# Kernel tuning notes

Hardware: AMD Instinct MI355X
Metric: run time of the kernel (lower is better)

Reference implementation:

```python
import jax, jax.numpy as jnp
import numpy as np

B_IN, B_L1, B_L2 = 64, 16, 8
F1, F2, F_OUT = 64, 128, 10
BATCH = 16
CPLX = jnp.complex64

# ---------- numpy precompute: quadrature weights, Wigner-d matrices, grids ----------

def _dh_weights(b):
    # Driscoll-Healy quadrature weights over the 2b beta samples
    j = np.arange(2 * b)
    l = np.arange(b)
    s = np.sin(np.outer(2 * j + 1, 2 * l + 1) * np.pi / (4 * b)) @ (1.0 / (2 * l + 1))
    return ((2.0 / b) * np.sin(np.pi * (2 * j + 1) / (4 * b)) * s).astype(np.float32)

def _wigner_d_all(lmax, betas):
    # d^l(beta) = exp(-i beta Jy) via eigendecomposition of Jy (quantum convention)
    betas = np.asarray(betas, np.float64)
    out = []
    for l in range(lmax + 1):
        m = np.arange(-l, l)
        cp = np.sqrt(l * (l + 1) - m * (m + 1))
        Jy = np.zeros((2 * l + 1, 2 * l + 1), np.complex128)
        Jy[np.arange(1, 2 * l + 1), np.arange(0, 2 * l)] = -0.5j * cp
        Jy[np.arange(0, 2 * l), np.arange(1, 2 * l + 1)] = 0.5j * cp
        lam, V = np.linalg.eigh(Jy)
        ph = np.exp(-1j * np.outer(betas, lam))
        d = np.einsum('mk,bk,nk->bmn', V, ph, V.conj())
        out.append(np.ascontiguousarray(d.real.astype(np.float32)))
    return out

def _s2_grid():
    beta = np.arange(1, 4) * (np.pi / 8) / 3
    alpha = np.linspace(0, 2 * np.pi, 8, endpoint=False)
    B, A = np.meshgrid(beta, alpha, indexing='ij')
    return B.ravel(), A.ravel()

def _so3_grid():
    beta = np.arange(1, 4) * (np.pi / 8) / 3
    alpha = np.linspace(0, 2 * np.pi, 8, endpoint=False)
    pre_gamma = np.linspace(0, 2 * np.pi, 8, endpoint=False)
    B, A, C = np.meshgrid(beta, alpha, pre_gamma, indexing='ij')
    return B.ravel(), A.ravel(), (C - A).ravel()

_BETAS_IN = np.pi * (2 * np.arange(2 * B_IN) + 1) / (4 * B_IN)
_BETAS_L1 = np.pi * (2 * np.arange(2 * B_L1) + 1) / (4 * B_L1)
_BETAS_L2 = np.pi * (2 * np.arange(2 * B_L2) + 1) / (4 * B_L2)
_W_IN = jnp.asarray(_dh_weights(B_IN))
_W_L1 = jnp.asarray(_dh_weights(B_L1))
_W_L2 = jnp.asarray(_dh_weights(B_L2))
_D_IN = _wigner_d_all(B_L1 - 1, _BETAS_IN)
_D_L1 = _wigner_d_all(B_L1 - 1, _BETAS_L1)
_D_L2 = _wigner_d_all(B_L2 - 1, _BETAS_L2)
_GB2, _GA2 = _s2_grid()
_GB3, _GA3, _GC3 = _so3_grid()
_D_G2 = _wigner_d_all(B_L1 - 1, _GB2)
_D_G3 = _wigner_d_all(B_L2 - 1, _GB3)

# spherical-harmonic / Wigner-D basis evaluated at kernel grid points
_PSI_S2 = []
for l in range(B_L1):
    m = np.arange(-l, l + 1)
    _PSI_S2.append(jnp.asarray((_D_G2[l][:, :, l].T * np.exp(-1j * np.outer(m, _GA2))).astype(np.complex64)))
_PSI_SO3 = []
for l in range(B_L2):
    m = np.arange(-l, l + 1)
    em = np.exp(-1j * np.outer(m, _GA3))
    en = np.exp(-1j * np.outer(m, _GC3))
    _PSI_SO3.append(jnp.asarray((_D_G3[l].transpose(1, 2, 0) * em[:, None, :] * en[None, :, :]).astype(np.complex64)))
_DCOL_IN = [jnp.asarray(_D_IN[l][:, :, l]) for l in range(B_L1)]  # d^l_{m,0}(beta_k)
_D_L1_J = [jnp.asarray(d) for d in _D_L1]
_D_L2_J = [jnp.asarray(d) for d in _D_L2]

# ---------- jax forward ----------

def _s2_fft(x):
    # x: [batch, f, 2b_in, 2b_in] (beta, alpha) -> list over l of [2l+1, batch, f] complex
    n = 2 * B_IN
    xf = jnp.fft.fft(x.astype(CPLX), axis=-1)  # e^{-i m alpha}
    out = []
    for l in range(B_L1):
        mi = np.arange(-l, l + 1) % n
        Xl = xf[..., mi]  # [batch, f, 2b, 2l+1]
        out.append(jnp.einsum('k,km,bfkm->mbf', _W_IN, _DCOL_IN[l], Xl) * (2 * np.pi / n))
    return out

def _so3_ifft(Fz, d_list, b):
    # Fz: list over l of [2l+1, 2l+1, batch, f] -> real [batch, f, 2b, 2b, 2b] (beta,alpha,gamma)
    n = 2 * b
    batch, f = Fz[0].shape[2], Fz[0].shape[3]
    S = jnp.zeros((batch, f, n, n, n), CPLX)
    for l in range(b):
        mi = np.arange(-l, l + 1) % n
        C = (2 * l + 1) * jnp.einsum('kmn,mnbf->bfkmn', d_list[l].astype(CPLX), Fz[l])
        S = S.at[:, :, :, mi[:, None], mi[None, :]].add(C)
    return jnp.real(jnp.fft.ifft2(S, axes=(-2, -1))) * (n * n)  # e^{+i m alpha} e^{+i n gamma}

def _so3_fft(x, d_list, w, b_l):
    # x: [batch, f, 2b, 2b, 2b] real -> list over l<b_l of [2l+1, 2l+1, batch, f] complex
    n = x.shape[-1]
    xf = jnp.fft.fft2(x.astype(CPLX), axes=(-2, -1)) / (n * n)
    out = []
    for l in range(b_l):
        mi = np.arange(-l, l + 1) % n
        Xl = xf[:, :, :, mi[:, None], mi[None, :]]  # [batch, f, 2b, 2l+1, 2l+1]
        out.append(jnp.einsum('k,kmn,bfkmn->mnbf', w, d_list[l], Xl) * (2 * np.pi))
    return out

def _forward(x, w1, w2, lin_w, lin_b):
    # S2Convolution: spectral x spectral-kernel outer product per degree l
    Fx = _s2_fft(x)
    Fy = [jnp.einsum('iog,mg->mio', w1.astype(CPLX), p) for p in _PSI_S2]
    Fz = [jnp.einsum('mbi,nio->mnbo', Fx[l], jnp.conj(Fy[l])) for l in range(B_L1)]
    y1 = jax.nn.relu(_so3_ifft(Fz, _D_L1_J, B_L1))
    # SO3Convolution
    Fx2 = _so3_fft(y1, _D_L1_J, _W_L1, B_L2)
    Fy2 = [jnp.einsum('iog,mng->mnio', w2.astype(CPLX), p) for p in _PSI_SO3]
    Fz2 = [jnp.einsum('mkbi,nkio->mnbo', Fx2[l], jnp.conj(Fy2[l])) for l in range(B_L2)]
    y2 = jax.nn.relu(_so3_ifft(Fz2, _D_L2_J, B_L2))
    # so3_integrate: quadrature over beta, uniform mean over alpha,gamma
    feat = jnp.einsum('k,bfk->bf', _W_L2, y2.mean(axis=(-2, -1)))
    return feat @ lin_w.T + lin_b


def setup_inputs() -> dict:
    key = jax.random.key(0)
    k1, k2, k3, k4 = jax.random.split(key, 4)
    x = jax.random.normal(k1, (BATCH, 1, 2 * B_IN, 2 * B_IN), jnp.float32)
    w1 = jax.random.normal(k2, (1, F1, 24), jnp.float32) / np.float32(np.sqrt(24))
    w2 = jax.random.normal(k3, (F1, F2, 192), jnp.float32) / np.float32(np.sqrt(192 * F1))
    lin_w = jax.random.normal(k4, (F_OUT, F2), jnp.float32) / np.float32(np.sqrt(F2))
    lin_b = jnp.zeros((F_OUT,), jnp.float32)
    return {'x': x, 'w1': w1, 'w2': w2, 'lin_w': lin_w, 'lin_b': lin_b}


def reference(x, w1, w2, lin_w, lin_b):
    return _forward(x, w1, w2, lin_w, lin_b)
```

## Files before the change

### kernel.cpp

```cpp
#include <hip/hip_runtime.h>
#include <cmath>
#include <vector>
#include <algorithm>

enum : int {
  OFF_WIN  = 0,
  OFF_WL1  = 128,
  OFF_WL2  = 160,
  OFF_DCOL = 176,
  OFF_D1A  = OFF_DCOL + 32768,
  OFF_D1B  = OFF_D1A + 174592,
  OFF_D2   = OFF_D1B + 174592,
  OFF_PSI2 = OFF_D2 + 10880,
  OFF_PSI3 = OFF_PSI2 + 12288,
  CONST_TOTAL = OFF_PSI3 + 261120
};

static constexpr size_t OFS_XF1  = 0;
static constexpr size_t OFS_FX   = 507904;
static constexpr size_t OFS_FY1  = 540672;
static constexpr size_t OFS_FX2  = 671744;
static constexpr size_t OFS_FY2  = 6242304;
static constexpr size_t OFS_FZ2  = 50806784;
static constexpr size_t OFS_W2T  = OFS_FZ2;
static constexpr size_t OFS_FEAT = 61947904;
static constexpr size_t WS_NEEDED = 61956096;

static inline int off3h(int l){ return (4*l*l*l - l)/3; }

namespace {

double fact_[32];
void init_fact(){ fact_[0]=1.0; for(int i=1;i<32;i++) fact_[i]=fact_[i-1]*i; }

void wigner_d(int l, double beta, double* d){
  int n = 2*l+1;
  double cb = std::cos(beta*0.5), sb = std::sin(beta*0.5);
  for(int r=0;r<n;r++){ int mp = r-l;
    for(int c=0;c<n;c++){ int m = c-l;
      double f = std::sqrt(fact_[l+mp]*fact_[l-mp]*fact_[l+m]*fact_[l-m]);
      int s0 = std::max(0, m-mp), s1 = std::min(l+m, l-mp);
      double sum = 0;
      for(int s=s0;s<=s1;s++){
        double t = (((mp-m+s)&1)? -1.0 : 1.0)
                 / (fact_[l+m-s]*fact_[s]*fact_[mp-m+s]*fact_[l-mp-s]);
        t *= std::pow(cb, (double)(2*l+m-mp-2*s)) * std::pow(sb, (double)(mp-m+2*s));
        sum += t;
      }
      d[r*n+c] = f*sum;
    }
  }
}

void dh_weights(int b, double* w){
  for(int j=0;j<2*b;j++){
    double s = 0;
    for(int l=0;l<b;l++) s += std::sin((2.0*j+1)*(2.0*l+1)*M_PI/(4.0*b))/(2.0*l+1);
    w[j] = (2.0/b)*std::sin(M_PI*(2.0*j+1)/(4.0*b))*s;
  }
}

float* g_const = nullptr;

struct ConstInit {
  ConstInit(){
    init_fact();
    std::vector<float> h((size_t)CONST_TOTAL, 0.0f);
    std::vector<double> tmp(31*31);
    std::vector<double> wl1(32);
    { std::vector<double> w(128); dh_weights(64, w.data()); for(int i=0;i<128;i++) h[OFF_WIN+i]=(float)w[i]; }
    { dh_weights(16, wl1.data()); for(int i=0;i<32;i++)  h[OFF_WL1+i]=(float)wl1[i]; }
    { std::vector<double> w(16);  dh_weights(8,  w.data()); for(int i=0;i<16;i++)  h[OFF_WL2+i]=(float)w[i]; }
    for(int l=0;l<16;l++){ int n=2*l+1;
      for(int k=0;k<128;k++){
        wigner_d(l, M_PI*(2.0*k+1)/256.0, tmp.data());
        for(int mi=0;mi<n;mi++) h[OFF_DCOL + (size_t)(l*l+mi)*128 + k] = (float)tmp[mi*n + l];
      }
    }
    for(int l=0;l<16;l++){ int n=2*l+1;
      for(int k=0;k<32;k++){
        wigner_d(l, M_PI*(2.0*k+1)/64.0, tmp.data());
        for(int t=0;t<n*n;t++){
          size_t base = (size_t)(off3h(l)+t)*32 + k;
          h[OFF_D1A + base] = (float)((2*l+1)*tmp[t]);
          if(l < 8)
            h[OFF_D1B + base] = (float)(2.0*M_PI*wl1[k]*tmp[t]/1024.0);
        }
      }
    }
    for(int l=0;l<8;l++){ int n=2*l+1;
      for(int k=0;k<16;k++){
        wigner_d(l, M_PI*(2.0*k+1)/32.0, tmp.data());
        for(int t=0;t<n*n;t++) h[OFF_D2 + (size_t)off3h(l)*16 + (size_t)k*n*n + t] = (float)tmp[t];
      }
    }
    for(int l=0;l<16;l++){ int n=2*l+1;
      for(int i=0;i<3;i++){
        wigner_d(l, (i+1)*(M_PI/8.0)/3.0, tmp.data());
        for(int j=0;j<8;j++){
          double alpha = 2.0*M_PI*j/8.0;
          int g = i*8+j;
          for(int mi=0;mi<n;mi++){
            double d = tmp[mi*n + l];
            double th = (double)(mi-l)*alpha;
            size_t base = OFF_PSI2 + ((size_t)(l*l+mi)*24 + g)*2;
            h[base+0] = (float)( d*std::cos(th));
            h[base+1] = (float)(-d*std::sin(th));
          }
        }
      }
    }
    for(int l=0;l<8;l++){ int n=2*l+1;
      for(int i=0;i<3;i++){
        wigner_d(l, (i+1)*(M_PI/8.0)/3.0, tmp.data());
        for(int j=0;j<8;j++){
          double alpha = 2.0*M_PI*j/8.0;
          for(int kk=0;kk<8;kk++){
            double gamma = 2.0*M_PI*kk/8.0 - alpha;
            int g = (i*8+j)*8+kk;
            for(int mi=0;mi<n;mi++) for(int ni=0;ni<n;ni++){
              double d = tmp[mi*n+ni];
              double th = (double)(mi-l)*alpha + (double)(ni-l)*gamma;
              size_t base = OFF_PSI3 + (((size_t)off3h(l)+ (size_t)mi*n+ni)*192 + g)*2;
              h[base+0] = (float)( d*std::cos(th));
              h[base+1] = (float)(-d*std::sin(th));
            }
          }
        }
      }
    }
    hipMalloc((void**)&g_const, sizeof(float)*(size_t)CONST_TOTAL);
    hipMemcpy(g_const, h.data(), sizeof(float)*(size_t)CONST_TOTAL, hipMemcpyHostToDevice);
  }
};
ConstInit g_init_;

}

__device__ __forceinline__ int off3d(int l){ return (4*l*l*l - l)/3; }
constexpr float TWO_PI_F = 6.28318530717958647692f;

__device__ __forceinline__ unsigned int f2bf(float f){
  union { float f; unsigned int u; } v; v.f = f;
  unsigned int r = v.u + 0x7FFFu + ((v.u >> 16) & 1u);
  return r >> 16;
}
__device__ __forceinline__ unsigned int pk2(float2 v){
  return f2bf(v.x) | (f2bf(v.y) << 16);
}
__device__ __forceinline__ float bflo(unsigned int u){
  union { unsigned int u; float f; } c; c.u = u << 16; return c.f;
}
__device__ __forceinline__ float bfhi(unsigned int u){
  union { unsigned int u; float f; } c; c.u = u & 0xffff0000u; return c.f;
}

typedef __attribute__((ext_vector_type(8))) short bf16x8;
typedef __attribute__((ext_vector_type(4))) float f32x4;

__global__ void k_fft_alpha(const float* __restrict__ x, float2* __restrict__ xf1){
  __shared__ float row[128];
  __shared__ float2 w128[128];
  int r = blockIdx.x;
  int t = threadIdx.x;
  row[t] = x[(size_t)r*128 + t];
  float ang = (TWO_PI_F/128.0f)*t;
  w128[t] = make_float2(cosf(ang), sinf(ang));
  __syncthreads();
  if(t < 31){
    int m = t - 15;
    float2 acc = make_float2(0.f,0.f);
    for(int a=0;a<128;a++){
      float2 w = w128[(m*a)&127];
      acc.x += row[a]*w.x;
      acc.y -= row[a]*w.y;
    }
    xf1[(size_t)r*31 + t] = acc;
  }
}

__global__ void k_fx(const float* __restrict__ cst, const float2* __restrict__ xf1,
                     float2* __restrict__ FxP){
  int idx = blockIdx.x*blockDim.x + threadIdx.x;
  int c2 = idx >> 4, b = idx & 15;
  int l = 0; while((l+1)*(l+1) <= c2) l++;
  int m = (c2 - l*l) - l;
  const float* W  = cst + OFF_WIN;
  const float* DC = cst + OFF_DCOL + (size_t)c2*128;
  float2 acc = make_float2(0.f,0.f);
  for(int k=0;k<128;k++){
    float wv = W[k]*DC[k];
    float2 xv = xf1[((size_t)b*128+k)*31 + (m+15)];
    acc.x += wv*xv.x; acc.y += wv*xv.y;
  }
  float s = TWO_PI_F/128.0f;
  FxP[(size_t)c2*16+b] = make_float2(acc.x*s, acc.y*s);
}

__global__ void k_fy1(const float* __restrict__ cst, const float* __restrict__ w1,
                      float2* __restrict__ FyP){
  int idx = blockIdx.x*blockDim.x + threadIdx.x;
  int c2 = idx >> 6, o = idx & 63;
  const float2* psi = (const float2*)(cst + OFF_PSI2) + (size_t)c2*24;
  const float* w1r = w1 + (size_t)o*24;
  float2 acc = make_float2(0.f,0.f);
  for(int g=0;g<24;g++){
    float wv = w1r[g];
    float2 p = psi[g];
    acc.x += wv*p.x; acc.y += wv*p.y;
  }
  FyP[(size_t)c2*64+o] = acc;
}

__global__ void __launch_bounds__(256,4) k_conv1(const float* __restrict__ cst,
                                                 const float2* __restrict__ FxP,
                                                 const float2* __restrict__ FyP,
                                                 unsigned int* __restrict__ FxB){
  __shared__ __align__(16) char L[39936];
  float2* FxL = (float2*)L;
  float2* FyL = FxL + 256;
  float2* SB  = (float2*)(L + 4096);
  unsigned int* yBu = (unsigned int*)(L + 4096);
  float2* XfB = (float2*)(L + 4096);
  unsigned int* TBu = (unsigned int*)(L + 23936);
  float2* T2B = (float2*)(L + 23936);
  float2* acc2= (float2*)(L + 34176);
  float2* w32 = (float2*)(L + 39616);
  int*    o3T = (int*)(L + 39872);

  int b = blockIdx.x >> 6, o = blockIdx.x & 63;
  int tid = threadIdx.x;
  if(tid < 32){ float ang = (TWO_PI_F/32.0f)*tid; w32[tid] = make_float2(cosf(ang), sinf(ang)); }
  if(tid < 16){ int l = tid; o3T[l] = (4*l*l*l - l)/3; }
  FxL[tid] = FxP[(size_t)tid*16 + b];
  FyL[tid] = FyP[(size_t)tid*64 + o];
  for(int t=tid; t<680; t+=256) acc2[t] = make_float2(0.f,0.f);

  const float* D1A = cst + OFF_D1A;
  const float* D1B = cst + OFF_D1B;

  for(int kt=0; kt<8; kt++){
    int k0 = kt*4;
    __syncthreads();
    for(int t=tid; t<496; t+=256){
      int mi = t/31, niq = t - mi*31;
      int n = niq-15;
      int an = n<0?-n:n;
      int lmin = mi>an?mi:an;
      float2 s0={0,0},s1={0,0},s2={0,0},s3={0,0};
      for(int l=lmin;l<16;l++){
        int c = 2*l+1, l2 = l*l;
        float2 fx = FxL[l2+l+mi];
        float2 fy = FyL[l2+(n+l)];
        float zx = fx.x*fy.x + fx.y*fy.y;
        float zy = fx.y*fy.x - fx.x*fy.y;
        const float4* dp = (const float4*)(D1A + (((size_t)o3T[l] + (mi+l)*c + (n+l))<<5) + k0);
        float4 d0 = dp[0];
        s0.x += d0.x*zx; s0.y += d0.x*zy;
        s1.x += d0.y*zx; s1.y += d0.y*zy;
        s2.x += d0.z*zx; s2.y += d0.z*zy;
        s3.x += d0.w*zx; s3.y += d0.w*zy;
      }
      float2* sp = SB + (size_t)t*5;
      sp[0]=s0; sp[1]=s1; sp[2]=s2; sp[3]=s3;
    }
    __syncthreads();
    {
      int mi = tid >> 4, cp = tid & 15;
      float2 a0[4], a1[4];
      #pragma unroll
      for(int j=0;j<4;j++){ a0[j]=make_float2(0,0); a1[j]=make_float2(0,0); }
      float2 step = w32[cp];
      float2 wv = w32[(15*cp)&31];
      float2 cur = make_float2(wv.x, -wv.y);
      const float2* srow = SB + (size_t)(mi*31)*5;
      for(int nb=0; nb<31; nb++){
        float2 q0 = srow[nb*5+0], q1 = srow[nb*5+1], q2 = srow[nb*5+2], q3 = srow[nb*5+3];
        float px, py;
        bool odd = (nb & 1);
        #define K1STEP(QX,QY,J) \
          px = QX*cur.x - QY*cur.y; py = QX*cur.y + QY*cur.x; \
          a0[J].x += px; a0[J].y += py; \
          if(odd){ a1[J].x += px; a1[J].y += py; } else { a1[J].x -= px; a1[J].y -= py; }
        K1STEP(q0.x,q0.y,0) K1STEP(q1.x,q1.y,1)
        K1STEP(q2.x,q2.y,2) K1STEP(q3.x,q3.y,3)
        #undef K1STEP
        float nx = cur.x*step.x - cur.y*step.y;
        cur.y = cur.x*step.y + cur.y*step.x;
        cur.x = nx;
      }
      unsigned int* tp0 = TBu + (size_t)(mi*32+cp)*5;
      tp0[0]=pk2(a0[0]); tp0[1]=pk2(a0[1]); tp0[2]=pk2(a0[2]); tp0[3]=pk2(a0[3]);
      unsigned int* tp1 = TBu + (size_t)(mi*32+cp+16)*5;
      tp1[0]=pk2(a1[0]); tp1[1]=pk2(a1[1]); tp1[2]=pk2(a1[2]); tp1[3]=pk2(a1[3]);
    }
    __syncthreads();
    {
      int c = tid & 31, aq = tid >> 5;
      float y0[4],y1[4],y2[4],y3[4], t0x[4];
      {
        const unsigned int* t0p = TBu + (size_t)c*5;
        t0x[0]=bflo(t0p[0]); t0x[1]=bflo(t0p[1]); t0x[2]=bflo(t0p[2]); t0x[3]=bflo(t0p[3]);
      }
      #pragma unroll
      for(int j=0;j<4;j++){ y0[j]=0; y1[j]=0; y2[j]=0; y3[j]=0; }
      #pragma unroll
      for(int m=1;m<16;m++){
        float2 w = w32[(m*aq)&31];
        const unsigned int* tp = TBu + (size_t)(m*32+c)*5;
        unsigned int d0=tp[0], d1=tp[1], d2=tp[2], d3=tp[3];
        float tx[4] = {bflo(d0),bflo(d1),bflo(d2),bflo(d3)};
        float ty[4] = {bfhi(d0),bfhi(d1),bfhi(d2),bfhi(d3)};
        #pragma unroll
        for(int j=0;j<4;j++){
          float px = tx[j]*w.x - ty[j]*w.y;
          float py = tx[j]*w.y + ty[j]*w.x;
          y0[j] += px;
          int r = m & 3;
          if(r==0){ y1[j] += px; y3[j] += px; }
          else if(r==1){ y1[j] -= py; y3[j] += py; }
          else if(r==2){ y1[j] -= px; y3[j] -= px; }
          else { y1[j] += py; y3[j] -= py; }
          y2[j] += (m&1)? -px : px;
        }
      }
      #define YWRITE(A, YV) { \
        float v0 = t0x[0]+2.f*YV[0], v1 = t0x[1]+2.f*YV[1], v2 = t0x[2]+2.f*YV[2], v3 = t0x[3]+2.f*YV[3]; \
        v0 = v0>0?v0:0; v1 = v1>0?v1:0; v2 = v2>0?v2:0; v3 = v3>0?v3:0; \
        unsigned int* yp = yBu + ((size_t)(A)*32 + c)*3; \
        yp[0] = f2bf(v0) | (f2bf(v1)<<16); \
        yp[1] = f2bf(v2) | (f2bf(v3)<<16); }
      YWRITE(aq,    y0)
      YWRITE(aq+8,  y1)
      YWRITE(aq+16, y2)
      YWRITE(aq+24, y3)
      #undef YWRITE
    }
    __syncthreads();
    {
      int mp = tid >> 5, c4 = tid & 31;
      float2 t2[4];
      #pragma unroll
      for(int j=0;j<4;j++) t2[j]=make_float2(0,0);
      for(int a=0;a<32;a++){
        float2 w = w32[(mp*a)&31];
        const unsigned int* yp = yBu + ((size_t)a*32 + c4)*3;
        unsigned int d0 = yp[0], d1 = yp[1];
        float yv[4] = {bflo(d0), bfhi(d0), bflo(d1), bfhi(d1)};
        #pragma unroll
        for(int j=0;j<4;j++){
          t2[j].x += yv[j]*w.x;
          t2[j].y -= yv[j]*w.y;
        }
      }
      float2* tp = T2B + (size_t)(mp*32+c4)*5;
      tp[0]=t2[0]; tp[1]=t2[1]; tp[2]=t2[2]; tp[3]=t2[3];
    }
    __syncthreads();
    if(tid < 120){
      int mp = tid/15, npq = tid - mp*15;
      int np = npq-7;
      float2 xf[4];
      #pragma unroll
      for(int j=0;j<4;j++) xf[j]=make_float2(0,0);
      float2 wv = w32[np&31];
      float2 step = make_float2(wv.x, -wv.y);
      float2 cur = make_float2(1.f, 0.f);
      const float2* trow = T2B + (size_t)(mp*32)*5;
      for(int c=0;c<32;c++){
        float2 q0 = trow[c*5+0], q1 = trow[c*5+1], q2 = trow[c*5+2], q3 = trow[c*5+3];
        float tx[4] = {q0.x,q1.x,q2.x,q3.x};
        float ty[4] = {q0.y,q1.y,q2.y,q3.y};
        #pragma unroll
        for(int j=0;j<4;j++){
          xf[j].x += tx[j]*cur.x - ty[j]*cur.y;
          xf[j].y += tx[j]*cur.y + ty[j]*cur.x;
        }
        float nx = cur.x*step.x - cur.y*step.y;
        cur.y = cur.x*step.y + cur.y*step.x;
        cur.x = nx;
      }
      float2* xp = XfB + (size_t)tid*5;
      xp[0]=xf[0]; xp[1]=xf[1]; xp[2]=xf[2]; xp[3]=xf[3];
    }
    __syncthreads();
    if(tid < 225){
      int mi2 = tid/15, ni2 = tid - mi2*15;
      int mp = mi2-7, np = ni2-7;
      float2 xf[4];
      if(mp >= 0){
        const float2* xp = XfB + (size_t)(mp*15+ni2)*5;
        xf[0]=xp[0]; xf[1]=xp[1]; xf[2]=xp[2]; xf[3]=xp[3];
      } else {
        const float2* xp = XfB + (size_t)((-mp)*15+(14-ni2))*5;
        float2 q0=xp[0],q1=xp[1],q2=xp[2],q3=xp[3];
        xf[0]=make_float2(q0.x,-q0.y); xf[1]=make_float2(q1.x,-q1.y);
        xf[2]=make_float2(q2.x,-q2.y); xf[3]=make_float2(q3.x,-q3.y);
      }
      int am = mp<0?-mp:mp, an = np<0?-np:np;
      int lmin = am>an?am:an;
      for(int l=lmin;l<8;l++){
        int c2 = 2*l+1;
        int cidx = o3T[l] + (mp+l)*c2 + (np+l);
        const float4* dp = (const float4*)(D1B + (((size_t)cidx)<<5) + k0);
        float4 d0 = dp[0];
        float rx = d0.x*xf[0].x + d0.y*xf[1].x + d0.z*xf[2].x + d0.w*xf[3].x;
        float ry = d0.x*xf[0].y + d0.y*xf[1].y + d0.z*xf[2].y + d0.w*xf[3].y;
        float2 cur = acc2[cidx];
        cur.x += rx; cur.y += ry;
        acc2[cidx] = cur;
      }
    }
  }
  __syncthreads();
  for(int t=tid; t<680; t+=256){
    float2 v = acc2[t];
    unsigned int pk = f2bf(v.x) | (f2bf(v.y) << 16);
    FxB[(size_t)t*1024 + b*64 + o] = pk;
  }
}

__global__ void k_w2t(const float* __restrict__ w2, float* __restrict__ w2t){
  int idx = blockIdx.x*256 + threadIdx.x;
  int g = idx >> 13, q = idx & 8191;
  int i = q & 63, o = q >> 6;
  w2t[idx] = w2[((size_t)i*128 + o)*192 + g];
}

__global__ void __launch_bounds__(256) k_fy2(const float* __restrict__ cst,
                                             const float* __restrict__ w2t,
                                             unsigned int* __restrict__ FyB){
  __shared__ float2 psiL[8*192];
  int cg  = blockIdx.x >> 5;
  int iog = blockIdx.x & 31;
  int tid = threadIdx.x;
  int q   = iog*256 + tid;
  int i   = q & 63, o = q >> 6;
  const float2* psi = (const float2*)(cst + OFF_PSI3) + (size_t)cg*8*192;
  for(int t=tid; t<1536; t+=256) psiL[t] = psi[t];
  __syncthreads();
  float2 acc[8];
  #pragma unroll
  for(int j=0;j<8;j++) acc[j] = make_float2(0.f,0.f);
  for(int g=0;g<192;g++){
    float w = w2t[(size_t)g*8192 + q];
    #pragma unroll
    for(int j=0;j<8;j++){
      float2 p = psiL[j*192+g];
      acc[j].x += w*p.x; acc[j].y += w*p.y;
    }
  }
  #pragma unroll
  for(int j=0;j<8;j++){
    size_t base = (size_t)(cg*8+j)*16384;
    unsigned int r  = f2bf(acc[j].x);
    unsigned int im = f2bf(acc[j].y);
    unsigned int nim= f2bf(-acc[j].y);
    FyB[base + (size_t)(2*o  )*64 + i] = r  | (im << 16);
    FyB[base + (size_t)(2*o+1)*64 + i] = nim| (r  << 16);
  }
}

__global__ void __launch_bounds__(256) k_fz2(const unsigned int* __restrict__ FxB,
                                             const unsigned int* __restrict__ FyB,
                                             float* __restrict__ Fz2f){
  int p = blockIdx.x;
  int c, o3, q;
  if(p < 225)      { c=15; o3=455; q=p; }
  else if(p < 394) { c=13; o3=286; q=p-225; }
  else if(p < 515) { c=11; o3=165; q=p-394; }
  else if(p < 596) { c=9;  o3=84;  q=p-515; }
  else if(p < 645) { c=7;  o3=35;  q=p-596; }
  else if(p < 670) { c=5;  o3=10;  q=p-645; }
  else if(p < 679) { c=3;  o3=1;   q=p-670; }
  else             { c=1;  o3=0;   q=0; }
  int mi = q / c, ni = q - mi*c;

  int tid  = threadIdx.x;
  int lane = tid & 63, wv = tid >> 6;
  int m16  = lane & 15, quad = lane >> 4;

  int aoff = m16*128 + quad*8;
  int boff = (wv*64 + m16)*128 + quad*8;

  f32x4 acc0 = {0,0,0,0}, acc1 = {0,0,0,0}, acc2v = {0,0,0,0}, acc3 = {0,0,0,0};

  const unsigned short* FxS = (const unsigned short*)FxB;
  const unsigned short* FyS = (const unsigned short*)FyB;

  for(int kk=0; kk<c; kk++){
    const unsigned short* Arow = FxS + (size_t)(o3 + mi*c + kk)*2048;
    const unsigned short* Brow = FyS + (size_t)(o3 + ni*c + kk)*32768;
    #pragma unroll
    for(int ig=0; ig<4; ig++){
      bf16x8 af = *(const bf16x8*)(Arow + aoff + ig*32);
      bf16x8 b0 = *(const bf16x8*)(Brow + boff            + ig*32);
      bf16x8 b1 = *(const bf16x8*)(Brow + boff + 1*2048   + ig*32);
      bf16x8 b2 = *(const bf16x8*)(Brow + boff + 2*2048   + ig*32);
      bf16x8 b3 = *(const bf16x8*)(Brow + boff + 3*2048   + ig*32);
      acc0  = __builtin_amdgcn_mfma_f32_16x16x32_bf16(af, b0, acc0,  0,0,0);
      acc1  = __builtin_amdgcn_mfma_f32_16x16x32_bf16(af, b1, acc1,  0,0,0);
      acc2v = __builtin_amdgcn_mfma_f32_16x16x32_bf16(af, b2, acc2v, 0,0,0);
      acc3  = __builtin_amdgcn_mfma_f32_16x16x32_bf16(af, b3, acc3,  0,0,0);
    }
  }
  int coefC = o3 + mi*c + ni;
  float* dst = Fz2f + (size_t)coefC*4096;
  int npb = wv*64 + m16;
  #pragma unroll
  for(int r=0;r<4;r++){
    int b = quad*4 + r;
    dst[(size_t)b*256 + npb       ] = acc0[r];
    dst[(size_t)b*256 + npb + 16  ] = acc1[r];
    dst[(size_t)b*256 + npb + 32  ] = acc2v[r];
    dst[(size_t)b*256 + npb + 48  ] = acc3[r];
  }
}

__global__ void __launch_bounds__(256) k_slice2(const float* __restrict__ cst,
                                                const float2* __restrict__ Fz2P,
                                                float* __restrict__ featP){
  __shared__ float2 FzL[680];
  __shared__ float2 S2[225];
  __shared__ float2 TA[240];
  __shared__ float2 w16[16];
  __shared__ float red[256];
  int bo = blockIdx.x;
  int tid = threadIdx.x;
  if(tid < 16){ float ang = (TWO_PI_F/16.0f)*tid; w16[tid] = make_float2(cosf(ang), sinf(ang)); }
  for(int t=tid; t<680; t+=256) FzL[t] = Fz2P[(size_t)t*2048 + bo];
  __syncthreads();
  const float* D2  = cst + OFF_D2;
  const float* WL2 = cst + OFF_WL2;
  float part = 0.f;
  for(int k2=0;k2<16;k2++){
    if(tid < 225){
      int mi = tid/15, ni = tid%15;
      int m = mi-7, n = ni-7;
      int am = m<0?-m:m, an = n<0?-n:n;
      int lmin = am>an?am:an;
      float2 acc = make_float2(0.f,0.f);
      for(int l=lmin;l<8;l++){
        int c = 2*l+1; int o3 = off3d(l);
        float dv = D2[(size_t)o3*16 + (size_t)k2*c*c + (m+l)*c + (n+l)];
        float wgt = (float)(2*l+1)*dv;
        float2 fzv = FzL[o3 + (m+l)*c + (n+l)];
        acc.x += wgt*fzv.x; acc.y += wgt*fzv.y;
      }
      S2[tid] = acc;
    }
    __syncthreads();
    if(tid < 240){
      int mi = tid >> 4, c = tid & 15;
      float2 acc = make_float2(0.f,0.f);
      for(int ni=0;ni<15;ni++){
        float2 sv = S2[mi*15+ni];
        float2 w = w16[((ni-7)*c)&15];
        acc.x += sv.x*w.x - sv.y*w.y;
        acc.y += sv.x*w.y + sv.y*w.x;
      }
      TA[mi*16+c] = acc;
    }
    __syncthreads();
    {
      int a = tid >> 4, c = tid & 15;
      float acc = 0.f;
      for(int mi=0;mi<15;mi++){
        float2 tv = TA[mi*16+c];
        float2 w = w16[((mi-7)*a)&15];
        acc += tv.x*w.x - tv.y*w.y;
      }
      if(acc > 0.f) part += WL2[k2]*acc;
    }
    __syncthreads();
  }
  red[tid] = part;
  __syncthreads();
  for(int s=128;s>0;s>>=1){ if(tid<s) red[tid]+=red[tid+s]; __syncthreads(); }
  if(tid==0) featP[bo] = red[0]*(1.0f/256.0f);
}

__global__ void k_out(const float* __restrict__ featP, const float* __restrict__ lin_w,
                      const float* __restrict__ lin_b, float* __restrict__ out){
  int t = threadIdx.x;
  if(t < 160){
    int b = t/10, j = t%10;
    float acc = lin_b[j];
    for(int o=0;o<128;o++) acc += featP[b*128+o]*lin_w[j*128+o];
    out[t] = acc;
  }
}

extern "C" void kernel_launch(void* const* d_in, const int* in_sizes, int n_in,
                              void* d_out, int out_size, void* d_ws, size_t ws_size,
                              hipStream_t stream){
  const float* x     = (const float*)d_in[0];
  const float* w1    = (const float*)d_in[1];
  const float* w2    = (const float*)d_in[2];
  const float* lin_w = (const float*)d_in[3];
  const float* lin_b = (const float*)d_in[4];
  float* out = (float*)d_out;
  if(ws_size < WS_NEEDED) return;
  char* ws = (char*)d_ws;
  float2* xf1  = (float2*)(ws + OFS_XF1);
  float2* FxP  = (float2*)(ws + OFS_FX);
  float2* FyP  = (float2*)(ws + OFS_FY1);
  unsigned int* FxB = (unsigned int*)(ws + OFS_FX2);
  unsigned int* FyB = (unsigned int*)(ws + OFS_FY2);
  float2* Fz2P = (float2*)(ws + OFS_FZ2);
  float*  w2tP = (float*)(ws + OFS_W2T);
  float*  featP= (float*)(ws + OFS_FEAT);
  const float* cst = g_const;

  k_fft_alpha<<<2048, 128, 0, stream>>>(x, xf1);
  k_fx      <<<16,   256, 0, stream>>>(cst, xf1, FxP);
  k_fy1     <<<64,   256, 0, stream>>>(cst, w1, FyP);
  k_conv1   <<<1024, 256, 0, stream>>>(cst, FxP, FyP, FxB);
  k_w2t     <<<6144, 256, 0, stream>>>(w2, w2tP);
  k_fy2     <<<2720, 256, 0, stream>>>(cst, w2tP, FyB);
  k_fz2     <<<680,  256, 0, stream>>>(FxB, FyB, (float*)Fz2P);
  k_slice2  <<<2048, 256, 0, stream>>>(cst, Fz2P, featP);
  k_out     <<<1,    256, 0, stream>>>(featP, lin_w, lin_b, out);
}
```

Before: 620.5 us.

## Batch eight beta slices per pass in slice2 and split alpha FFT across threads

The Wigner-d table for the last layer is re-laid out so the 16 beta samples for each coefficient sit contiguously, with the (2l+1) factor folded in. k_slice2 now handles eight beta slices per pass with float4 loads, so each Fz coefficient load is reused eight times and the number of barriers drops. Shared scratch is padded to a stride of 9 to reduce bank conflicts. k_fft_alpha now has four thread groups each sum a quarter of the row and then combines them, instead of 31 threads doing all the work. The cost is more shared memory and more registers, which could lower occupancy.

```diff
diff --git a/kernel.cpp b/kernel.cpp
--- a/kernel.cpp
+++ b/kernel.cpp
@@ -91,7 +91,8 @@
     for(int l=0;l<8;l++){ int n=2*l+1;
       for(int k=0;k<16;k++){
         wigner_d(l, M_PI*(2.0*k+1)/32.0, tmp.data());
-        for(int t=0;t<n*n;t++) h[OFF_D2 + (size_t)off3h(l)*16 + (size_t)k*n*n + t] = (float)tmp[t];
+        for(int t=0;t<n*n;t++)
+          h[OFF_D2 + (size_t)(off3h(l)+t)*16 + k] = (float)((2*l+1)*tmp[t]);
       }
     }
     for(int l=0;l<16;l++){ int n=2*l+1;
@@ -161,21 +162,32 @@
 __global__ void k_fft_alpha(const float* __restrict__ x, float2* __restrict__ xf1){
   __shared__ float row[128];
   __shared__ float2 w128[128];
+  __shared__ float2 red2[4][31];
   int r = blockIdx.x;
   int t = threadIdx.x;
   row[t] = x[(size_t)r*128 + t];
   float ang = (TWO_PI_F/128.0f)*t;
   w128[t] = make_float2(cosf(ang), sinf(ang));
   __syncthreads();
-  if(t < 31){
-    int m = t - 15;
+  int mi = t & 31, part = t >> 5;
+  if(mi < 31){
+    int m = mi - 15;
     float2 acc = make_float2(0.f,0.f);
-    for(int a=0;a<128;a++){
+    int a0 = part*32;
+    for(int a=a0;a<a0+32;a++){
       float2 w = w128[(m*a)&127];
       acc.x += row[a]*w.x;
       acc.y -= row[a]*w.y;
     }
-    xf1[(size_t)r*31 + t] = acc;
+    red2[part][mi] = acc;
+  }
+  __syncthreads();
+  if(t < 31){
+    float2 s = red2[0][t];
+    float2 s1 = red2[1][t], s2 = red2[2][t], s3 = red2[3][t];
+    s.x += s1.x + s2.x + s3.x;
+    s.y += s1.y + s2.y + s3.y;
+    xf1[(size_t)r*31 + t] = s;
   }
 }
 
@@ -517,63 +529,92 @@
   }
 }
 
-__global__ void __launch_bounds__(256) k_slice2(const float* __restrict__ cst,
-                                                const float2* __restrict__ Fz2P,
-                                                float* __restrict__ featP){
+__global__ void __launch_bounds__(256,4) k_slice2(const float* __restrict__ cst,
+                                                  const float2* __restrict__ Fz2P,
+                                                  float* __restrict__ featP){
   __shared__ float2 FzL[680];
-  __shared__ float2 S2[225];
-  __shared__ float2 TA[240];
+  __shared__ float2 S2B[225*9];
+  __shared__ float2 TAB[240*9];
   __shared__ float2 w16[16];
   __shared__ float red[256];
   int bo = blockIdx.x;
   int tid = threadIdx.x;
   if(tid < 16){ float ang = (TWO_PI_F/16.0f)*tid; w16[tid] = make_float2(cosf(ang), sinf(ang)); }
   for(int t=tid; t<680; t+=256) FzL[t] = Fz2P[(size_t)t*2048 + bo];
-  __syncthreads();
   const float* D2  = cst + OFF_D2;
   const float* WL2 = cst + OFF_WL2;
   float part = 0.f;
-  for(int k2=0;k2<16;k2++){
+  __syncthreads();
+  for(int it=0; it<2; it++){
+    int k0 = it*8;
+    if(it) __syncthreads();
     if(tid < 225){
-      int mi = tid/15, ni = tid%15;
+      int mi = tid/15, ni = tid - mi*15;
       int m = mi-7, n = ni-7;
       int am = m<0?-m:m, an = n<0?-n:n;
       int lmin = am>an?am:an;
-      float2 acc = make_float2(0.f,0.f);
+      float2 a0={0,0},a1={0,0},a2={0,0},a3={0,0},a4={0,0},a5={0,0},a6={0,0},a7={0,0};
       for(int l=lmin;l<8;l++){
-        int c = 2*l+1; int o3 = off3d(l);
-        float dv = D2[(size_t)o3*16 + (size_t)k2*c*c + (m+l)*c + (n+l)];
-        float wgt = (float)(2*l+1)*dv;
-        float2 fzv = FzL[o3 + (m+l)*c + (n+l)];
-        acc.x += wgt*fzv.x; acc.y += wgt*fzv.y;
-      }
-      S2[tid] = acc;
+        int c2 = 2*l+1;
+        int idx = off3d(l) + (m+l)*c2 + (n+l);
+        const float4* dp = (const float4*)(D2 + ((size_t)idx<<4) + k0);
+        float4 d0 = dp[0], d1 = dp[1];
+        float2 fz = FzL[idx];
+        a0.x += d0.x*fz.x; a0.y += d0.x*fz.y;
+        a1.x += d0.y*fz.x; a1.y += d0.y*fz.y;
+        a2.x += d0.z*fz.x; a2.y += d0.z*fz.y;
+        a3.x += d0.w*fz.x; a3.y += d0.w*fz.y;
+        a4.x += d1.x*fz.x; a4.y += d1.x*fz.y;
+        a5.x += d1.y*fz.x; a5.y += d1.y*fz.y;
+        a6.x += d1.z*fz.x; a6.y += d1.z*fz.y;
+        a7.x += d1.w*fz.x; a7.y += d1.w*fz.y;
+      }
+      float2* sp = S2B + (size_t)tid*9;
+      sp[0]=a0; sp[1]=a1; sp[2]=a2; sp[3]=a3; sp[4]=a4; sp[5]=a5; sp[6]=a6; sp[7]=a7;
     }
     __syncthreads();
     if(tid < 240){
       int mi = tid >> 4, c = tid & 15;
-      float2 acc = make_float2(0.f,0.f);
+      float2 acc[8];
+      #pragma unroll
+      for(int j=0;j<8;j++) acc[j]=make_float2(0,0);
+      const float2* srow = S2B + (size_t)(mi*15)*9;
       for(int ni=0;ni<15;ni++){
-        float2 sv = S2[mi*15+ni];
         float2 w = w16[((ni-7)*c)&15];
-        acc.x += sv.x*w.x - sv.y*w.y;
-        acc.y += sv.x*w.y + sv.y*w.x;
-      }
-      TA[mi*16+c] = acc;
+        const float2* sp = srow + (size_t)ni*9;
+        #pragma unroll
+        for(int j=0;j<8;j++){
+          float2 s = sp[j];
+          acc[j].x += s.x*w.x - s.y*w.y;
+          acc[j].y += s.x*w.y + s.y*w.x;
+        }
+      }
+      float2* tp = TAB + (size_t)tid*9;
+      #pragma unroll
+      for(int j=0;j<8;j++) tp[j] = acc[j];
     }
     __syncthreads();
     {
       int a = tid >> 4, c = tid & 15;
-      float acc = 0.f;
+      float yv[8];
+      #pragma unroll
+      for(int j=0;j<8;j++) yv[j]=0.f;
       for(int mi=0;mi<15;mi++){
-        float2 tv = TA[mi*16+c];
         float2 w = w16[((mi-7)*a)&15];
-        acc += tv.x*w.x - tv.y*w.y;
-      }
-      if(acc > 0.f) part += WL2[k2]*acc;
-    }
-    __syncthreads();
-  }
+        const float2* tp = TAB + (size_t)(mi*16+c)*9;
+        #pragma unroll
+        for(int j=0;j<8;j++){
+          float2 tv = tp[j];
+          yv[j] += tv.x*w.x - tv.y*w.y;
+        }
+      }
+      #pragma unroll
+      for(int j=0;j<8;j++){
+        if(yv[j] > 0.f) part += WL2[k0+j]*yv[j];
+      }
+    }
+  }
+  __syncthreads();
   red[tid] = part;
   __syncthreads();
   for(int s=128;s>0;s>>=1){ if(tid<s) red[tid]+=red[tid+s]; __syncthreads(); }
```

New measurement: 1.141 ms. +83.9%, slower.

## Split alpha-FFT and Fx reductions across threads, re-layout D2, relax conv1 bounds

Applied to the files above, without the earlier changes.

k_fft_alpha now uses all 128 threads, each covering a quarter of the alpha samples, and combines the four partial sums through shared memory. Previously only 31 threads did the work. k_fx splits its k-loop across four thread groups with a shared reduction and launches four times as many blocks. The D2 table is stored k-innermost with the (2l+1) factor folded in on the host, which removes a multiply and gives simpler indexing in the slice kernel. k_conv1's launch bounds drop from 4 to 2 waves per SIMD, allowing more registers at the cost of occupancy.

```diff
diff --git a/kernel.cpp b/kernel.cpp
--- a/kernel.cpp
+++ b/kernel.cpp
@@ -91,7 +91,8 @@
     for(int l=0;l<8;l++){ int n=2*l+1;
       for(int k=0;k<16;k++){
         wigner_d(l, M_PI*(2.0*k+1)/32.0, tmp.data());
-        for(int t=0;t<n*n;t++) h[OFF_D2 + (size_t)off3h(l)*16 + (size_t)k*n*n + t] = (float)tmp[t];
+        for(int t=0;t<n*n;t++)
+          h[OFF_D2 + (size_t)(off3h(l)+t)*16 + k] = (float)((2*l+1)*tmp[t]);
       }
     }
     for(int l=0;l<16;l++){ int n=2*l+1;
@@ -161,40 +162,62 @@
 __global__ void k_fft_alpha(const float* __restrict__ x, float2* __restrict__ xf1){
   __shared__ float row[128];
   __shared__ float2 w128[128];
+  __shared__ float2 red2[4][31];
   int r = blockIdx.x;
   int t = threadIdx.x;
   row[t] = x[(size_t)r*128 + t];
   float ang = (TWO_PI_F/128.0f)*t;
   w128[t] = make_float2(cosf(ang), sinf(ang));
   __syncthreads();
-  if(t < 31){
-    int m = t - 15;
+  int mi = t & 31, part = t >> 5;
+  if(mi < 31){
+    int m = mi - 15;
     float2 acc = make_float2(0.f,0.f);
-    for(int a=0;a<128;a++){
+    int a0 = part*32;
+    for(int a=a0;a<a0+32;a++){
       float2 w = w128[(m*a)&127];
       acc.x += row[a]*w.x;
       acc.y -= row[a]*w.y;
     }
-    xf1[(size_t)r*31 + t] = acc;
+    red2[part][mi] = acc;
+  }
+  __syncthreads();
+  if(t < 31){
+    float2 s = red2[0][t];
+    float2 s1 = red2[1][t], s2 = red2[2][t], s3 = red2[3][t];
+    s.x += s1.x + s2.x + s3.x;
+    s.y += s1.y + s2.y + s3.y;
+    xf1[(size_t)r*31 + t] = s;
   }
 }
 
 __global__ void k_fx(const float* __restrict__ cst, const float2* __restrict__ xf1,
                      float2* __restrict__ FxP){
-  int idx = blockIdx.x*blockDim.x + threadIdx.x;
+  __shared__ float2 redL[256];
+  int lp = threadIdx.x & 63;
+  int kc = threadIdx.x >> 6;
+  int idx = blockIdx.x*64 + lp;
   int c2 = idx >> 4, b = idx & 15;
   int l = 0; while((l+1)*(l+1) <= c2) l++;
   int m = (c2 - l*l) - l;
   const float* W  = cst + OFF_WIN;
   const float* DC = cst + OFF_DCOL + (size_t)c2*128;
   float2 acc = make_float2(0.f,0.f);
-  for(int k=0;k<128;k++){
+  int k0 = kc*32;
+  for(int k=k0;k<k0+32;k++){
     float wv = W[k]*DC[k];
     float2 xv = xf1[((size_t)b*128+k)*31 + (m+15)];
     acc.x += wv*xv.x; acc.y += wv*xv.y;
   }
-  float s = TWO_PI_F/128.0f;
-  FxP[(size_t)c2*16+b] = make_float2(acc.x*s, acc.y*s);
+  redL[threadIdx.x] = acc;
+  __syncthreads();
+  if(kc == 0){
+    float2 p1 = redL[lp+64], p2 = redL[lp+128], p3 = redL[lp+192];
+    acc.x += p1.x + p2.x + p3.x;
+    acc.y += p1.y + p2.y + p3.y;
+    float s = TWO_PI_F/128.0f;
+    FxP[(size_t)c2*16+b] = make_float2(acc.x*s, acc.y*s);
+  }
 }
 
 __global__ void k_fy1(const float* __restrict__ cst, const float* __restrict__ w1,
@@ -212,7 +235,7 @@
   FyP[(size_t)c2*64+o] = acc;
 }
 
-__global__ void __launch_bounds__(256,4) k_conv1(const float* __restrict__ cst,
+__global__ void __launch_bounds__(256,2) k_conv1(const float* __restrict__ cst,
                                                  const float2* __restrict__ FxP,
                                                  const float2* __restrict__ FyP,
                                                  unsigned int* __restrict__ FxB){
@@ -541,11 +564,11 @@
       int lmin = am>an?am:an;
       float2 acc = make_float2(0.f,0.f);
       for(int l=lmin;l<8;l++){
-        int c = 2*l+1; int o3 = off3d(l);
-        float dv = D2[(size_t)o3*16 + (size_t)k2*c*c + (m+l)*c + (n+l)];
-        float wgt = (float)(2*l+1)*dv;
-        float2 fzv = FzL[o3 + (m+l)*c + (n+l)];
-        acc.x += wgt*fzv.x; acc.y += wgt*fzv.y;
+        int c = 2*l+1;
+        int idx = off3d(l) + (m+l)*c + (n+l);
+        float dv = D2[((size_t)idx<<4) + k2];
+        float2 fzv = FzL[idx];
+        acc.x += dv*fzv.x; acc.y += dv*fzv.y;
       }
       S2[tid] = acc;
     }
@@ -613,7 +636,7 @@
   const float* cst = g_const;
 
   k_fft_alpha<<<2048, 128, 0, stream>>>(x, xf1);
-  k_fx      <<<16,   256, 0, stream>>>(cst, xf1, FxP);
+  k_fx      <<<64,   256, 0, stream>>>(cst, xf1, FxP);
   k_fy1     <<<64,   256, 0, stream>>>(cst, w1, FyP);
   k_conv1   <<<1024, 256, 0, stream>>>(cst, FxP, FyP, FxB);
   k_w2t     <<<6144, 256, 0, stream>>>(w2, w2tP);
```

New measurement: 655.0 us. +5.6%, slower.
